# Optimization experiments

Hardware: AMD Instinct MI355X
Metric: run time of the kernel (lower is better)

Reference implementation:

```python
import jax, jax.numpy as jnp
import numpy as np
import math

N = 4096
D = 256


def _xavier(key, shape):
    fan_in, fan_out = shape[0], shape[1]
    std = math.sqrt(2.0 / (fan_in + fan_out))
    return jax.random.normal(key, shape, dtype=jnp.float32) * std


def setup_inputs() -> dict:
    key = jax.random.key(0)
    ks = jax.random.split(key, 12)
    return {
        "cur": jax.random.normal(ks[0], (N, D), dtype=jnp.float32),
        "pre": jax.random.normal(ks[1], (N, D), dtype=jnp.float32),
        # SpatialHyperedge params
        "r_proj_s": _xavier(ks[2], (D, D)),
        "incidence_s": _xavier(ks[3], (N, N - 1)),
        # TemporalHyperedge params
        "r_proj_t": _xavier(ks[4], (D, D)),
        "incidence_t": _xavier(ks[5], (N, N)),
        # HHNodeMP params
        "node_proj": _xavier(ks[6], (D, D)),
        "spa_edge_proj": _xavier(ks[7], (D, D)),
        "tmp_edge_proj": _xavier(ks[8], (D, D)),
        "theta_w": _xavier(ks[9], (D, D)),
        "theta_b": jnp.zeros((D,), dtype=jnp.float32),
    }


def _scatter_slave(vals):
    """Place [N, N-1] per-row slave values into a zero-diagonal [N, N] matrix.
    Row i's k-th slave is column k if k < i else k+1 (all j != i in order)."""
    n = vals.shape[0]
    k = jnp.arange(n - 1)[None, :]
    cols = k + (k >= jnp.arange(n)[:, None])  # [N, N-1] column indices
    rows = jnp.broadcast_to(jnp.arange(n)[:, None], (n, n - 1))
    return jnp.zeros((n, n), dtype=vals.dtype).at[rows.reshape(-1), cols.reshape(-1)].set(vals.reshape(-1))


def _fro(x):
    return jnp.sqrt(jnp.sum(x * x))


def reference(cur, pre, r_proj_s, incidence_s, r_proj_t, incidence_t,
              node_proj, spa_edge_proj, tmp_edge_proj, theta_w, theta_b):
    n, d = cur.shape
    inv_sqrt_d = 1.0 / math.sqrt(d)

    # ---- SpatialHyperedge ----
    Xd = jax.lax.stop_gradient(cur)
    master_s = Xd @ r_proj_s                                   # [N, D]
    M_s_full = _scatter_slave(incidence_s)                     # [N, N], zero diag
    neigh_recon_s = M_s_full @ Xd                              # == bmm over gathered slaves
    spatial_loss = (_fro(master_s - neigh_recon_s) * 0.2
                    + jnp.sum(jnp.abs(incidence_s))
                    + 0.001 * _fro(incidence_s))
    # clamp(min=0) then zero-out entries not strictly > 0  => relu-like
    clipped_s = jnp.where(incidence_s > 0.0, incidence_s, 0.0)
    incidence_all = _scatter_slave(clipped_s) + jnp.eye(n, dtype=cur.dtype)

    # ---- TemporalHyperedge ----
    cur_d = jax.lax.stop_gradient(cur)
    pre_d = jax.lax.stop_gradient(pre)
    master_t = cur_d @ r_proj_t
    neigh_recon_t = incidence_t @ pre_d
    temporal_loss = (_fro(master_t - neigh_recon_t) * 0.2
                     + jnp.sum(jnp.abs(incidence_t))
                     + 0.001 * _fro(incidence_t))
    incidence_t_clipped = jnp.maximum(incidence_t, 0.0)

    # ---- SpatialHyperedgeMP ----
    spa_edge_fea = incidence_all @ cur
    spa_deg = jnp.sum(incidence_all, axis=1, keepdims=True)
    spa_emb = spa_edge_fea / spa_deg                           # [N, D]

    # ---- TemporalHyperedgeMP ----
    tmp_edge_fea = incidence_t_clipped @ pre + cur
    tmp_deg = jnp.sum(incidence_t_clipped, axis=1, keepdims=True) + 1.0
    tmp_emb = tmp_edge_fea / tmp_deg                           # [N, D]

    # ---- HHNodeMP ----
    node_fea = cur @ node_proj
    spa_fea = spa_emb @ spa_edge_proj
    tmp_fea = tmp_emb @ tmp_edge_proj
    spa_attn = jnp.sum(spa_fea * node_fea, axis=1, keepdims=True) * inv_sqrt_d
    tmp_attn = jnp.sum(tmp_fea * node_fea, axis=1, keepdims=True) * inv_sqrt_d
    val = spa_attn * spa_fea + tmp_attn * tmp_fea
    node_emb = jax.nn.relu(val @ theta_w.T + theta_b)          # dropout = identity (eval)

    return node_emb, temporal_loss + spatial_loss
```

## Files before the change

### kernel.cpp

```cpp
#include <hip/hip_runtime.h>
#include <hip/hip_bf16.h>
#include <math.h>

#define NN 4096
#define DD 256

typedef __bf16 bf16x8 __attribute__((ext_vector_type(8)));
typedef short  short8 __attribute__((ext_vector_type(8)));
typedef float  f32x4  __attribute__((ext_vector_type(4)));

#define MFMA16(a, b, c) __builtin_amdgcn_mfma_f32_16x16x32_bf16((a), (b), (c), 0, 0, 0)

__device__ inline bf16x8 brelu(bf16x8 a) {
    short8 s = __builtin_bit_cast(short8, a);
    s = s & ~(s >> 15);
    return __builtin_bit_cast(bf16x8, s);
}

__device__ inline float wave_red(float v) {
#pragma unroll
    for (int o = 32; o > 0; o >>= 1) v += __shfl_down(v, o, 64);
    return v;
}

__device__ inline unsigned short bfbits(float f) {
    return __builtin_bit_cast(unsigned short, (__bf16)f);
}

__global__ __launch_bounds__(256) void k_prep(const float* __restrict__ cur,
                                              const float* __restrict__ pre,
                                              __bf16* __restrict__ cur_bf,
                                              __bf16* __restrict__ curT,
                                              __bf16* __restrict__ preT) {
    const int z = blockIdx.z;
    const int i0 = blockIdx.x * 64, d0 = blockIdx.y * 64;
    const float* src = z ? pre : cur;
    __bf16* dstT = z ? preT : curT;
    __shared__ unsigned short tile[64][72];
    const int t = threadIdx.x;
    const int r = t >> 2, c4 = (t & 3) * 16;
    const float* srow = src + (size_t)(i0 + r) * DD + d0 + c4;
    alignas(16) unsigned short loc[16];
#pragma unroll
    for (int e = 0; e < 4; ++e) {
        float4 v = ((const float4*)srow)[e];
        loc[e * 4 + 0] = bfbits(v.x);
        loc[e * 4 + 1] = bfbits(v.y);
        loc[e * 4 + 2] = bfbits(v.z);
        loc[e * 4 + 3] = bfbits(v.w);
    }
#pragma unroll
    for (int e = 0; e < 16; ++e) tile[r][c4 + e] = loc[e];
    if (z == 0) {
        __bf16* drow = cur_bf + (size_t)(i0 + r) * DD + d0 + c4;
        *(uint4*)drow = *(uint4*)&loc[0];
        *(uint4*)(drow + 8) = *(uint4*)&loc[8];
    }
    __syncthreads();
    alignas(16) unsigned short o[16];
#pragma unroll
    for (int e = 0; e < 16; ++e) o[e] = tile[c4 + e][r];
    __bf16* trow = dstT + (size_t)(d0 + r) * NN + i0 + c4;
    *(uint4*)trow = *(uint4*)&o[0];
    *(uint4*)(trow + 8) = *(uint4*)&o[8];
}

__global__ __launch_bounds__(256) void k_proj(
    const float* __restrict__ a0, const float* __restrict__ a1, const float* __restrict__ a2,
    const float* __restrict__ a3, const float* __restrict__ a4, const float* __restrict__ a5,
    __bf16* __restrict__ o0, __bf16* __restrict__ o1, __bf16* __restrict__ o2,
    __bf16* __restrict__ o3, __bf16* __restrict__ o4, __bf16* __restrict__ o5) {
    const int id = blockIdx.y, r = blockIdx.x, t = threadIdx.x;
    const float* src = id == 0 ? a0 : id == 1 ? a1 : id == 2 ? a2 : id == 3 ? a3 : id == 4 ? a4 : a5;
    __bf16* dst = id == 0 ? o0 : id == 1 ? o1 : id == 2 ? o2 : id == 3 ? o3 : id == 4 ? o4 : o5;
    float v = src[r * DD + t];
    if (id < 5) dst[t * DD + r] = (__bf16)v;
    else        dst[r * DD + t] = (__bf16)v;
}

__global__ __launch_bounds__(256) void k_conv_t(const float* __restrict__ inc,
                                                __bf16* __restrict__ Mbf,
                                                float* __restrict__ rowsum,
                                                float* __restrict__ pAbs, float* __restrict__ pSq) {
    const int i = blockIdx.x, t = threadIdx.x;
    const float4* src = (const float4*)(inc + (size_t)i * NN);
    ushort4* dst = (ushort4*)(Mbf + (size_t)i * NN);
    float rs = 0.f, as = 0.f, qs = 0.f;
#pragma unroll
    for (int e = 0; e < 4; ++e) {
        const int f = t + 256 * e;
        float4 v = src[f];
        float x[4] = {v.x, v.y, v.z, v.w};
        unsigned short o[4];
#pragma unroll
        for (int j = 0; j < 4; ++j) {
            float fv = x[j];
            as += fabsf(fv); qs += fv * fv; rs += fmaxf(fv, 0.f);
            o[j] = bfbits(fv);
        }
        dst[f] = make_ushort4(o[0], o[1], o[2], o[3]);
    }
    __shared__ float red[3][4];
    const int w = t >> 6, lane = t & 63;
    rs = wave_red(rs); as = wave_red(as); qs = wave_red(qs);
    if (lane == 0) { red[0][w] = rs; red[1][w] = as; red[2][w] = qs; }
    __syncthreads();
    if (t == 0) {
        rowsum[i] = red[0][0] + red[0][1] + red[0][2] + red[0][3];
        pAbs[i]   = red[1][0] + red[1][1] + red[1][2] + red[1][3];
        pSq[i]    = red[2][0] + red[2][1] + red[2][2] + red[2][3];
    }
}

__global__ __launch_bounds__(256) void k_conv_s(const float* __restrict__ inc,
                                                __bf16* __restrict__ Mbf,
                                                float* __restrict__ rowsum,
                                                float* __restrict__ pAbs, float* __restrict__ pSq) {
    const int i = blockIdx.x, t = threadIdx.x;
    __shared__ unsigned short row[NN];
    const float* srow = inc + (size_t)i * (NN - 1);
    float rs = 0.f, as = 0.f, qs = 0.f;
#pragma unroll
    for (int e = 0; e < 4; ++e) {
        const int f = t + 256 * e;
        float x[4] = {0.f, 0.f, 0.f, 0.f};
        if (f < 1023) __builtin_memcpy(x, srow + 4 * f, 16);
        else          __builtin_memcpy(x, srow + 4092, 12);
#pragma unroll
        for (int j = 0; j < 4; ++j) {
            const int k = 4 * f + j;
            float fv = x[j];
            as += fabsf(fv); qs += fv * fv; rs += fmaxf(fv, 0.f);
            if (k < NN - 1) row[k + (k >= i)] = bfbits(fv);
        }
    }
    if (t == 0) row[i] = 0;
    __syncthreads();
    uint4* dOut = (uint4*)(Mbf + (size_t)i * NN);
    const uint4* sIn = (const uint4*)row;
    dOut[t] = sIn[t];
    dOut[t + 256] = sIn[t + 256];
    __shared__ float red[3][4];
    const int w = t >> 6, lane = t & 63;
    rs = wave_red(rs); as = wave_red(as); qs = wave_red(qs);
    if (lane == 0) { red[0][w] = rs; red[1][w] = as; red[2][w] = qs; }
    __syncthreads();
    if (t == 0) {
        rowsum[i] = red[0][0] + red[0][1] + red[0][2] + red[0][3];
        pAbs[i]   = red[1][0] + red[1][1] + red[1][2] + red[1][3];
        pSq[i]    = red[2][0] + red[2][1] + red[2][2] + red[2][3];
    }
}

template <int DUAL>
__device__ inline void mfma_step(const __bf16 (&As)[64][72], const __bf16 (&Bs)[64][72],
                                 int wr, int wc, int quad, int l16,
                                 f32x4 (&accR)[2][2], f32x4 (&accL)[2][2]) {
#pragma unroll
    for (int ks = 0; ks < 2; ++ks) {
        const int kc = ks * 32 + quad * 8;
        bf16x8 a0 = *(const bf16x8*)&As[wr * 32 + l16][kc];
        bf16x8 a1 = *(const bf16x8*)&As[wr * 32 + 16 + l16][kc];
        bf16x8 b0 = *(const bf16x8*)&Bs[wc * 32 + l16][kc];
        bf16x8 b1 = *(const bf16x8*)&Bs[wc * 32 + 16 + l16][kc];
        accR[0][0] = MFMA16(a0, b0, accR[0][0]);
        accR[0][1] = MFMA16(a0, b1, accR[0][1]);
        accR[1][0] = MFMA16(a1, b0, accR[1][0]);
        accR[1][1] = MFMA16(a1, b1, accR[1][1]);
        if (DUAL) {
            bf16x8 a0r = brelu(a0), a1r = brelu(a1);
            accL[0][0] = MFMA16(a0r, b0, accL[0][0]);
            accL[0][1] = MFMA16(a0r, b1, accL[0][1]);
            accL[1][0] = MFMA16(a1r, b0, accL[1][0]);
            accL[1][1] = MFMA16(a1r, b1, accL[1][1]);
        }
    }
}

__global__ __launch_bounds__(256) void k_big(const __bf16* __restrict__ Mt, const __bf16* __restrict__ Ms,
                                             const __bf16* __restrict__ preT, const __bf16* __restrict__ curT,
                                             const float* __restrict__ negMt, const float* __restrict__ negMs,
                                             const float* __restrict__ cur,
                                             const float* __restrict__ rsT, const float* __restrict__ rsS,
                                             __bf16* __restrict__ embT, __bf16* __restrict__ embS,
                                             float* __restrict__ pDiff) {
    const int flat = blockIdx.x + 4 * (blockIdx.y + 64 * blockIdx.z);
    const int swz = (flat & 7) * 64 + (flat >> 3);
    const int bx = swz & 3, by = (swz >> 2) & 63, z = swz >> 8;
    const __bf16* A  = z ? Ms : Mt;
    const __bf16* BT = z ? curT : preT;
    const float* negM = z ? negMs : negMt;
    const float* rs   = z ? rsS : rsT;
    __bf16* emb       = z ? embS : embT;
    const int n0 = bx * 64, m0 = by * 64;
    __shared__ __bf16 As[2][64][72], Bs[2][64][72];
    __shared__ float sred[4];
    f32x4 accR[2][2], accL[2][2];
#pragma unroll
    for (int i = 0; i < 2; ++i)
#pragma unroll
        for (int j = 0; j < 2; ++j) { accR[i][j] = (f32x4)0.f; accL[i][j] = (f32x4)0.f; }
    const int t = threadIdx.x, w = t >> 6, lane = t & 63, quad = lane >> 4, l16 = lane & 15;
    const int wr = w >> 1, wc = w & 1;
    const int sr = t >> 2, sc = (t & 3) * 16;
    const __bf16* gA = A + (size_t)(m0 + sr) * NN + sc;
    const __bf16* gB = BT + (size_t)(n0 + sr) * NN + sc;
    uint4 av0 = *(const uint4*)(gA);
    uint4 av1 = *(const uint4*)(gA + 8);
    uint4 bv0 = *(const uint4*)(gB);
    uint4 bv1 = *(const uint4*)(gB + 8);
    gA += 64; gB += 64;
    *(uint4*)&As[0][sr][sc] = av0; *(uint4*)&As[0][sr][sc + 8] = av1;
    *(uint4*)&Bs[0][sr][sc] = bv0; *(uint4*)&Bs[0][sr][sc + 8] = bv1;
    av0 = *(const uint4*)(gA);
    av1 = *(const uint4*)(gA + 8);
    bv0 = *(const uint4*)(gB);
    bv1 = *(const uint4*)(gB + 8);
    gA += 64; gB += 64;
    __builtin_amdgcn_sched_barrier(0);
    asm volatile("s_waitcnt lgkmcnt(0)" ::: "memory");
    __builtin_amdgcn_s_barrier();
    int c = 0;
    for (int kt = 0; kt < NN / 64; ++kt) {
        __builtin_amdgcn_s_setprio(1);
        mfma_step<1>(As[c], Bs[c], wr, wc, quad, l16, accR, accL);
        __builtin_amdgcn_s_setprio(0);
        if (kt < NN / 64 - 1) {
            *(uint4*)&As[c ^ 1][sr][sc] = av0; *(uint4*)&As[c ^ 1][sr][sc + 8] = av1;
            *(uint4*)&Bs[c ^ 1][sr][sc] = bv0; *(uint4*)&Bs[c ^ 1][sr][sc + 8] = bv1;
            if (kt < NN / 64 - 2) {
                av0 = *(const uint4*)(gA);
                av1 = *(const uint4*)(gA + 8);
                bv0 = *(const uint4*)(gB);
                bv1 = *(const uint4*)(gB + 8);
                gA += 64; gB += 64;
            }
            __builtin_amdgcn_sched_barrier(0);
            asm volatile("s_waitcnt lgkmcnt(0)" ::: "memory");
        }
        __builtin_amdgcn_s_barrier();
        c ^= 1;
    }
    float sumd = 0.f;
#pragma unroll
    for (int mi = 0; mi < 2; ++mi)
#pragma unroll
        for (int ni = 0; ni < 2; ++ni)
#pragma unroll
            for (int r = 0; r < 4; ++r) {
                int gr = m0 + wr * 32 + mi * 16 + quad * 4 + r;
                int gc = n0 + wc * 32 + ni * 16 + l16;
                size_t idx = (size_t)gr * DD + gc;
                float diff = accR[mi][ni][r] + negM[idx];
                sumd += diff * diff;
                float inv = 1.f / (rs[gr] + 1.f);
                emb[idx] = (__bf16)((accL[mi][ni][r] + cur[idx]) * inv);
            }
    sumd = wave_red(sumd);
    if (lane == 0) sred[w] = sumd;
    __syncthreads();
    if (t == 0)
        pDiff[z * 256 + by * 4 + bx] = sred[0] + sred[1] + sred[2] + sred[3];
}

__global__ __launch_bounds__(256) void k_small3(const __bf16* __restrict__ cur_bf,
                                                const __bf16* __restrict__ pTs, const __bf16* __restrict__ pTt,
                                                const __bf16* __restrict__ pTn,
                                                float* __restrict__ negMs, float* __restrict__ negMt,
                                                float* __restrict__ nodeFea) {
    const int z = blockIdx.z;
    const __bf16* BT = z == 0 ? pTs : (z == 1 ? pTt : pTn);
    const int n0 = blockIdx.x * 64, m0 = blockIdx.y * 64;
    __shared__ __bf16 As[64][72], Bs[64][72];
    f32x4 accR[2][2];
#pragma unroll
    for (int i = 0; i < 2; ++i)
#pragma unroll
        for (int j = 0; j < 2; ++j) accR[i][j] = (f32x4)0.f;
    const int t = threadIdx.x, w = t >> 6, lane = t & 63, quad = lane >> 4, l16 = lane & 15;
    const int wr = w >> 1, wc = w & 1;
    const int sr = t >> 2, sc = (t & 3) * 16;
    const __bf16* gA = cur_bf + (size_t)(m0 + sr) * DD + sc;
    const __bf16* gB = BT + (size_t)(n0 + sr) * DD + sc;
    for (int kt = 0; kt < DD / 64; ++kt) {
        uint4 av0 = *(const uint4*)(gA);
        uint4 av1 = *(const uint4*)(gA + 8);
        uint4 bv0 = *(const uint4*)(gB);
        uint4 bv1 = *(const uint4*)(gB + 8);
        __syncthreads();
        *(uint4*)&As[sr][sc] = av0; *(uint4*)&As[sr][sc + 8] = av1;
        *(uint4*)&Bs[sr][sc] = bv0; *(uint4*)&Bs[sr][sc + 8] = bv1;
        __syncthreads();
        mfma_step<0>(As, Bs, wr, wc, quad, l16, accR, accR);
        gA += 64; gB += 64;
    }
#pragma unroll
    for (int mi = 0; mi < 2; ++mi)
#pragma unroll
        for (int ni = 0; ni < 2; ++ni)
#pragma unroll
            for (int r = 0; r < 4; ++r) {
                int gr = m0 + wr * 32 + mi * 16 + quad * 4 + r;
                int gc = n0 + wc * 32 + ni * 16 + l16;
                size_t idx = (size_t)gr * DD + gc;
                float v = accR[mi][ni][r];
                if (z == 0) negMs[idx] = -v;
                else if (z == 1) negMt[idx] = -v;
                else nodeFea[idx] = v;
            }
}

__global__ __launch_bounds__(256) void k_fea(const __bf16* __restrict__ embS, const __bf16* __restrict__ embT,
                                             const __bf16* __restrict__ pTspa, const __bf16* __restrict__ pTtmp,
                                             float* __restrict__ spaF, float* __restrict__ tmpF) {
    const int z = blockIdx.z;
    const __bf16* Ae = z ? embT : embS;
    const __bf16* BT = z ? pTtmp : pTspa;
    float* outF = z ? tmpF : spaF;
    const int n0 = blockIdx.x * 64, m0 = blockIdx.y * 64;
    __shared__ __bf16 As[64][72], Bs[64][72];
    f32x4 accR[2][2];
#pragma unroll
    for (int i = 0; i < 2; ++i)
#pragma unroll
        for (int j = 0; j < 2; ++j) accR[i][j] = (f32x4)0.f;
    const int t = threadIdx.x, w = t >> 6, lane = t & 63, quad = lane >> 4, l16 = lane & 15;
    const int wr = w >> 1, wc = w & 1;
    const int sr = t >> 2, sc = (t & 3) * 16;
    const __bf16* gA = Ae + (size_t)(m0 + sr) * DD + sc;
    const __bf16* gB = BT + (size_t)(n0 + sr) * DD + sc;
    for (int kt = 0; kt < DD / 64; ++kt) {
        uint4 av0 = *(const uint4*)(gA);
        uint4 av1 = *(const uint4*)(gA + 8);
        uint4 bv0 = *(const uint4*)(gB);
        uint4 bv1 = *(const uint4*)(gB + 8);
        __syncthreads();
        *(uint4*)&As[sr][sc] = av0; *(uint4*)&As[sr][sc + 8] = av1;
        *(uint4*)&Bs[sr][sc] = bv0; *(uint4*)&Bs[sr][sc + 8] = bv1;
        __syncthreads();
        mfma_step<0>(As, Bs, wr, wc, quad, l16, accR, accR);
        gA += 64; gB += 64;
    }
#pragma unroll
    for (int mi = 0; mi < 2; ++mi)
#pragma unroll
        for (int ni = 0; ni < 2; ++ni)
#pragma unroll
            for (int r = 0; r < 4; ++r) {
                int gr = m0 + wr * 32 + mi * 16 + quad * 4 + r;
                int gc = n0 + wc * 32 + ni * 16 + l16;
                outF[(size_t)gr * DD + gc] = accR[mi][ni][r];
            }
}

__global__ __launch_bounds__(256) void k_attn(const float* __restrict__ spaF, const float* __restrict__ tmpF,
                                              const float* __restrict__ nodeF,
                                              float* __restrict__ spaA, float* __restrict__ tmpA) {
    const int t = threadIdx.x, w = t >> 6, lane = t & 63;
    const int i = blockIdx.x * 4 + w;
    const float4* sf = (const float4*)(spaF + (size_t)i * DD);
    const float4* tf = (const float4*)(tmpF + (size_t)i * DD);
    const float4* nf = (const float4*)(nodeF + (size_t)i * DD);
    float4 s = sf[lane], p = tf[lane], n = nf[lane];
    float ds = s.x * n.x + s.y * n.y + s.z * n.z + s.w * n.w;
    float dt = p.x * n.x + p.y * n.y + p.z * n.z + p.w * n.w;
    ds = wave_red(ds); dt = wave_red(dt);
    if (lane == 0) { spaA[i] = ds * 0.0625f; tmpA[i] = dt * 0.0625f; }
}

__global__ __launch_bounds__(256) void k_final(const float* __restrict__ spaF, const float* __restrict__ tmpF,
                                               const float* __restrict__ spaA, const float* __restrict__ tmpA,
                                               const __bf16* __restrict__ thetaBf, const float* __restrict__ thetaB,
                                               float* __restrict__ out) {
    const int n0 = blockIdx.x * 64, m0 = blockIdx.y * 64;
    __shared__ __bf16 As[64][72], Bs[64][72];
    f32x4 accR[2][2];
#pragma unroll
    for (int i = 0; i < 2; ++i)
#pragma unroll
        for (int j = 0; j < 2; ++j) accR[i][j] = (f32x4)0.f;
    const int t = threadIdx.x, w = t >> 6, lane = t & 63, quad = lane >> 4, l16 = lane & 15;
    const int wr = w >> 1, wc = w & 1;
    const int sr = t >> 2, sc = (t & 3) * 16;
    const float sa = spaA[m0 + sr], ta = tmpA[m0 + sr];
    const float* gS = spaF + (size_t)(m0 + sr) * DD + sc;
    const float* gT = tmpF + (size_t)(m0 + sr) * DD + sc;
    const __bf16* gB = thetaBf + (size_t)(n0 + sr) * DD + sc;
    for (int kt = 0; kt < DD / 64; ++kt) {
        __bf16 tmp[16];
#pragma unroll
        for (int e4 = 0; e4 < 4; ++e4) {
            float4 vs = ((const float4*)gS)[e4];
            float4 vt = ((const float4*)gT)[e4];
            tmp[e4 * 4 + 0] = (__bf16)(sa * vs.x + ta * vt.x);
            tmp[e4 * 4 + 1] = (__bf16)(sa * vs.y + ta * vt.y);
            tmp[e4 * 4 + 2] = (__bf16)(sa * vs.z + ta * vt.z);
            tmp[e4 * 4 + 3] = (__bf16)(sa * vs.w + ta * vt.w);
        }
        uint4 bv0 = *(const uint4*)(gB);
        uint4 bv1 = *(const uint4*)(gB + 8);
        __syncthreads();
        *(uint4*)&As[sr][sc] = *(uint4*)&tmp[0]; *(uint4*)&As[sr][sc + 8] = *(uint4*)&tmp[8];
        *(uint4*)&Bs[sr][sc] = bv0; *(uint4*)&Bs[sr][sc + 8] = bv1;
        __syncthreads();
        mfma_step<0>(As, Bs, wr, wc, quad, l16, accR, accR);
        gS += 64; gT += 64; gB += 64;
    }
#pragma unroll
    for (int mi = 0; mi < 2; ++mi)
#pragma unroll
        for (int ni = 0; ni < 2; ++ni)
#pragma unroll
            for (int r = 0; r < 4; ++r) {
                int gr = m0 + wr * 32 + mi * 16 + quad * 4 + r;
                int gc = n0 + wc * 32 + ni * 16 + l16;
                float v = accR[mi][ni][r] + thetaB[gc];
                out[(size_t)gr * DD + gc] = fmaxf(v, 0.f);
            }
}

__global__ __launch_bounds__(256) void k_loss(const float* __restrict__ pAbsT, const float* __restrict__ pSqT,
                                              const float* __restrict__ pAbsS, const float* __restrict__ pSqS,
                                              const float* __restrict__ pDiff,
                                              float* __restrict__ out) {
    const int t = threadIdx.x;
    float aT = 0.f, qT = 0.f, aS = 0.f, qS = 0.f;
#pragma unroll
    for (int j = 0; j < 16; ++j) {
        const int i = t + 256 * j;
        aT += pAbsT[i]; qT += pSqT[i]; aS += pAbsS[i]; qS += pSqS[i];
    }
    float dT = pDiff[t], dS = pDiff[256 + t];
    aT = wave_red(aT); qT = wave_red(qT); aS = wave_red(aS); qS = wave_red(qS);
    dT = wave_red(dT); dS = wave_red(dS);
    __shared__ float red[6][4];
    const int w = t >> 6, lane = t & 63;
    if (lane == 0) { red[0][w] = aT; red[1][w] = qT; red[2][w] = aS; red[3][w] = qS; red[4][w] = dT; red[5][w] = dS; }
    __syncthreads();
    if (t == 0) {
        float s[6];
#pragma unroll
        for (int k = 0; k < 6; ++k) s[k] = red[k][0] + red[k][1] + red[k][2] + red[k][3];
        float l = s[0] + 0.001f * sqrtf(s[1]) + 0.2f * sqrtf(s[4])
                + s[2] + 0.001f * sqrtf(s[3]) + 0.2f * sqrtf(s[5]);
        out[(size_t)NN * DD] = l;
    }
}

extern "C" void kernel_launch(void* const* d_in, const int* in_sizes, int n_in,
                              void* d_out, int out_size, void* d_ws, size_t ws_size,
                              hipStream_t stream) {
    (void)in_sizes; (void)n_in; (void)out_size; (void)ws_size;
    const float* cur      = (const float*)d_in[0];
    const float* pre      = (const float*)d_in[1];
    const float* r_proj_s = (const float*)d_in[2];
    const float* inc_s    = (const float*)d_in[3];
    const float* r_proj_t = (const float*)d_in[4];
    const float* inc_t    = (const float*)d_in[5];
    const float* node_pj  = (const float*)d_in[6];
    const float* spa_pj   = (const float*)d_in[7];
    const float* tmp_pj   = (const float*)d_in[8];
    const float* theta_w  = (const float*)d_in[9];
    const float* theta_b  = (const float*)d_in[10];
    float* out = (float*)d_out;

    char* p = (char*)d_ws;
    auto alloc = [&](size_t bytes) -> void* {
        void* r = (void*)p;
        p += (bytes + 255) & ~(size_t)255;
        return r;
    };
    __bf16* Mt      = (__bf16*)alloc((size_t)NN * NN * 2);
    __bf16* Ms      = (__bf16*)alloc((size_t)NN * NN * 2);
    __bf16* cur_bf  = (__bf16*)alloc((size_t)NN * DD * 2);
    __bf16* curT    = (__bf16*)alloc((size_t)NN * DD * 2);
    __bf16* preT    = (__bf16*)alloc((size_t)NN * DD * 2);
    __bf16* pTs     = (__bf16*)alloc((size_t)DD * DD * 2);
    __bf16* pTt     = (__bf16*)alloc((size_t)DD * DD * 2);
    __bf16* pTn     = (__bf16*)alloc((size_t)DD * DD * 2);
    __bf16* pTspa   = (__bf16*)alloc((size_t)DD * DD * 2);
    __bf16* pTtmp   = (__bf16*)alloc((size_t)DD * DD * 2);
    __bf16* thetaBf = (__bf16*)alloc((size_t)DD * DD * 2);
    __bf16* embS    = (__bf16*)alloc((size_t)NN * DD * 2);
    __bf16* embT    = (__bf16*)alloc((size_t)NN * DD * 2);
    float* negMs    = (float*)alloc((size_t)NN * DD * 4);
    float* negMt    = (float*)alloc((size_t)NN * DD * 4);
    float* nodeFea  = (float*)alloc((size_t)NN * DD * 4);
    float* spaF     = (float*)alloc((size_t)NN * DD * 4);
    float* tmpF     = (float*)alloc((size_t)NN * DD * 4);
    float* rsS      = (float*)alloc((size_t)NN * 4);
    float* rsT      = (float*)alloc((size_t)NN * 4);
    float* spaA     = (float*)alloc((size_t)NN * 4);
    float* tmpA     = (float*)alloc((size_t)NN * 4);
    float* pAbsT    = (float*)alloc((size_t)NN * 4);
    float* pSqT     = (float*)alloc((size_t)NN * 4);
    float* pAbsS    = (float*)alloc((size_t)NN * 4);
    float* pSqS     = (float*)alloc((size_t)NN * 4);
    float* pDiff    = (float*)alloc(512 * 4);

    k_prep<<<dim3(NN / 64, DD / 64, 2), 256, 0, stream>>>(cur, pre, cur_bf, curT, preT);
    k_proj<<<dim3(DD, 6), 256, 0, stream>>>(r_proj_s, r_proj_t, node_pj, spa_pj, tmp_pj, theta_w,
                                            pTs, pTt, pTn, pTspa, pTtmp, thetaBf);
    k_conv_t<<<NN, 256, 0, stream>>>(inc_t, Mt, rsT, pAbsT, pSqT);
    k_conv_s<<<NN, 256, 0, stream>>>(inc_s, Ms, rsS, pAbsS, pSqS);
    k_small3<<<dim3(4, 64, 3), 256, 0, stream>>>(cur_bf, pTs, pTt, pTn, negMs, negMt, nodeFea);
    k_big<<<dim3(4, 64, 2), 256, 0, stream>>>(Mt, Ms, preT, curT, negMt, negMs, cur,
                                              rsT, rsS, embT, embS, pDiff);
    k_fea<<<dim3(4, 64, 2), 256, 0, stream>>>(embS, embT, pTspa, pTtmp, spaF, tmpF);
    k_attn<<<NN / 4, 256, 0, stream>>>(spaF, tmpF, nodeFea, spaA, tmpA);
    k_final<<<dim3(4, 64), 256, 0, stream>>>(spaF, tmpF, spaA, tmpA, thetaBf, theta_b, out);
    k_loss<<<1, 256, 0, stream>>>(pAbsT, pSqT, pAbsS, pSqS, pDiff, out);
}
```

Measured before the change: 262.2 us.

## Use direct global-to-LDS loads with XOR swizzle in k_big; fuse attention dot into k_fea

The main big GEMM kernel now stages A/B tiles via global_load_lds directly into an XOR-swizzled, unpadded LDS buffer. It prefetches two tiles ahead with vmcnt-based waits and reads fragments into registers before issuing the next stage. This removes register staging and the ds_write traffic in the K loop. Separately, the attention dot products are computed in the k_fea epilogue as per-slice partial sums reduced in k_final, which eliminates the k_attn launch and its reread of spaF, tmpF and nodeFea.

```diff
diff --git a/kernel.cpp b/kernel.cpp
--- a/kernel.cpp
+++ b/kernel.cpp
@@ -8,6 +8,10 @@
 typedef __bf16 bf16x8 __attribute__((ext_vector_type(8)));
 typedef short  short8 __attribute__((ext_vector_type(8)));
 typedef float  f32x4  __attribute__((ext_vector_type(4)));
+
+typedef __attribute__((address_space(1))) const void gv_t;
+typedef __attribute__((address_space(3))) void lv_t;
+#define GLD16(gp, lp) __builtin_amdgcn_global_load_lds((gv_t*)(gp), (lv_t*)(lp), 16, 0, 0)
 
 #define MFMA16(a, b, c) __builtin_amdgcn_mfma_f32_16x16x32_bf16((a), (b), (c), 0, 0, 0)
 
@@ -152,10 +156,9 @@
     }
 }
 
-template <int DUAL>
-__device__ inline void mfma_step(const __bf16 (&As)[64][72], const __bf16 (&Bs)[64][72],
-                                 int wr, int wc, int quad, int l16,
-                                 f32x4 (&accR)[2][2], f32x4 (&accL)[2][2]) {
+__device__ inline void mfma_step_s(const __bf16 (&As)[64][72], const __bf16 (&Bs)[64][72],
+                                   int wr, int wc, int quad, int l16,
+                                   f32x4 (&accR)[2][2]) {
 #pragma unroll
     for (int ks = 0; ks < 2; ++ks) {
         const int kc = ks * 32 + quad * 8;
@@ -167,13 +170,6 @@
         accR[0][1] = MFMA16(a0, b1, accR[0][1]);
         accR[1][0] = MFMA16(a1, b0, accR[1][0]);
         accR[1][1] = MFMA16(a1, b1, accR[1][1]);
-        if (DUAL) {
-            bf16x8 a0r = brelu(a0), a1r = brelu(a1);
-            accL[0][0] = MFMA16(a0r, b0, accL[0][0]);
-            accL[0][1] = MFMA16(a0r, b1, accL[0][1]);
-            accL[1][0] = MFMA16(a1r, b0, accL[1][0]);
-            accL[1][1] = MFMA16(a1r, b1, accL[1][1]);
-        }
     }
 }
 
@@ -193,7 +189,7 @@
     const float* rs   = z ? rsS : rsT;
     __bf16* emb       = z ? embS : embT;
     const int n0 = bx * 64, m0 = by * 64;
-    __shared__ __bf16 As[2][64][72], Bs[2][64][72];
+    __shared__ __bf16 sm[2][2][64][64];
     __shared__ float sred[4];
     f32x4 accR[2][2], accL[2][2];
 #pragma unroll
@@ -202,43 +198,66 @@
         for (int j = 0; j < 2; ++j) { accR[i][j] = (f32x4)0.f; accL[i][j] = (f32x4)0.f; }
     const int t = threadIdx.x, w = t >> 6, lane = t & 63, quad = lane >> 4, l16 = lane & 15;
     const int wr = w >> 1, wc = w & 1;
-    const int sr = t >> 2, sc = (t & 3) * 16;
-    const __bf16* gA = A + (size_t)(m0 + sr) * NN + sc;
-    const __bf16* gB = BT + (size_t)(n0 + sr) * NN + sc;
-    uint4 av0 = *(const uint4*)(gA);
-    uint4 av1 = *(const uint4*)(gA + 8);
-    uint4 bv0 = *(const uint4*)(gB);
-    uint4 bv1 = *(const uint4*)(gB + 8);
-    gA += 64; gB += 64;
-    *(uint4*)&As[0][sr][sc] = av0; *(uint4*)&As[0][sr][sc + 8] = av1;
-    *(uint4*)&Bs[0][sr][sc] = bv0; *(uint4*)&Bs[0][sr][sc + 8] = bv1;
-    av0 = *(const uint4*)(gA);
-    av1 = *(const uint4*)(gA + 8);
-    bv0 = *(const uint4*)(gB);
-    bv1 = *(const uint4*)(gB + 8);
-    gA += 64; gB += 64;
+    const int lr = lane >> 3, lc = lane & 7;
+    const int q0 = 2 * w, q1 = q0 + 1;
+    const int csw = ((lc ^ lr) * 8);
+    const __bf16* gA0 = A + (size_t)(m0 + 8 * q0 + lr) * NN + csw;
+    const __bf16* gA1 = A + (size_t)(m0 + 8 * q1 + lr) * NN + csw;
+    const __bf16* gB0 = BT + (size_t)(n0 + 8 * q0 + lr) * NN + csw;
+    const __bf16* gB1 = BT + (size_t)(n0 + 8 * q1 + lr) * NN + csw;
+    auto stage = [&](int b, int tk) {
+        const int ko = tk * 64;
+        GLD16(gA0 + ko, &sm[b][0][8 * q0][0]);
+        GLD16(gA1 + ko, &sm[b][0][8 * q1][0]);
+        GLD16(gB0 + ko, &sm[b][1][8 * q0][0]);
+        GLD16(gB1 + ko, &sm[b][1][8 * q1][0]);
+    };
+    stage(0, 0);
+    stage(1, 1);
+    asm volatile("s_waitcnt vmcnt(4)" ::: "memory");
+    __builtin_amdgcn_s_barrier();
     __builtin_amdgcn_sched_barrier(0);
-    asm volatile("s_waitcnt lgkmcnt(0)" ::: "memory");
-    __builtin_amdgcn_s_barrier();
+    const int h8 = l16 & 7;
+    const int ra0 = wr * 32 + l16, ra1 = ra0 + 16;
+    const int rb0 = wc * 32 + l16, rb1 = rb0 + 16;
     int c = 0;
-    for (int kt = 0; kt < NN / 64; ++kt) {
+    const int NT = NN / 64;
+    for (int kt = 0; kt < NT; ++kt) {
+        bf16x8 a0k[2], a1k[2], b0k[2], b1k[2];
+#pragma unroll
+        for (int ks = 0; ks < 2; ++ks) {
+            const int sw = ((4 * ks + quad) ^ h8) * 8;
+            a0k[ks] = *(const bf16x8*)&sm[c][0][ra0][sw];
+            a1k[ks] = *(const bf16x8*)&sm[c][0][ra1][sw];
+            b0k[ks] = *(const bf16x8*)&sm[c][1][rb0][sw];
+            b1k[ks] = *(const bf16x8*)&sm[c][1][rb1][sw];
+        }
+        asm volatile("s_waitcnt lgkmcnt(0)" ::: "memory");
+        __builtin_amdgcn_sched_barrier(0);
+        __builtin_amdgcn_s_barrier();
+        __builtin_amdgcn_sched_barrier(0);
+        if (kt < NT - 2) stage(c, kt + 2);
+        __builtin_amdgcn_sched_barrier(0);
         __builtin_amdgcn_s_setprio(1);
-        mfma_step<1>(As[c], Bs[c], wr, wc, quad, l16, accR, accL);
+#pragma unroll
+        for (int ks = 0; ks < 2; ++ks) {
+            accR[0][0] = MFMA16(a0k[ks], b0k[ks], accR[0][0]);
+            accR[0][1] = MFMA16(a0k[ks], b1k[ks], accR[0][1]);
+            accR[1][0] = MFMA16(a1k[ks], b0k[ks], accR[1][0]);
+            accR[1][1] = MFMA16(a1k[ks], b1k[ks], accR[1][1]);
+            bf16x8 a0r = brelu(a0k[ks]), a1r = brelu(a1k[ks]);
+            accL[0][0] = MFMA16(a0r, b0k[ks], accL[0][0]);
+            accL[0][1] = MFMA16(a0r, b1k[ks], accL[0][1]);
+            accL[1][0] = MFMA16(a1r, b0k[ks], accL[1][0]);
+            accL[1][1] = MFMA16(a1r, b1k[ks], accL[1][1]);
+        }
         __builtin_amdgcn_s_setprio(0);
-        if (kt < NN / 64 - 1) {
-            *(uint4*)&As[c ^ 1][sr][sc] = av0; *(uint4*)&As[c ^ 1][sr][sc + 8] = av1;
-            *(uint4*)&Bs[c ^ 1][sr][sc] = bv0; *(uint4*)&Bs[c ^ 1][sr][sc + 8] = bv1;
-            if (kt < NN / 64 - 2) {
-                av0 = *(const uint4*)(gA);
-                av1 = *(const uint4*)(gA + 8);
-                bv0 = *(const uint4*)(gB);
-                bv1 = *(const uint4*)(gB + 8);
-                gA += 64; gB += 64;
-            }
+        if (kt < NT - 1) {
+            if (kt < NT - 2) asm volatile("s_waitcnt vmcnt(4)" ::: "memory");
+            else             asm volatile("s_waitcnt vmcnt(0)" ::: "memory");
+            __builtin_amdgcn_s_barrier();
             __builtin_amdgcn_sched_barrier(0);
-            asm volatile("s_waitcnt lgkmcnt(0)" ::: "memory");
-        }
-        __builtin_amdgcn_s_barrier();
+        }
         c ^= 1;
     }
     float sumd = 0.f;
@@ -291,7 +310,7 @@
         *(uint4*)&As[sr][sc] = av0; *(uint4*)&As[sr][sc + 8] = av1;
         *(uint4*)&Bs[sr][sc] = bv0; *(uint4*)&Bs[sr][sc + 8] = bv1;
         __syncthreads();
-        mfma_step<0>(As, Bs, wr, wc, quad, l16, accR, accR);
+        mfma_step_s(As, Bs, wr, wc, quad, l16, accR);
         gA += 64; gB += 64;
     }
 #pragma unroll
@@ -312,11 +331,14 @@
 
 __global__ __launch_bounds__(256) void k_fea(const __bf16* __restrict__ embS, const __bf16* __restrict__ embT,
                                              const __bf16* __restrict__ pTspa, const __bf16* __restrict__ pTtmp,
-                                             float* __restrict__ spaF, float* __restrict__ tmpF) {
+                                             const float* __restrict__ nodeF,
+                                             float* __restrict__ spaF, float* __restrict__ tmpF,
+                                             float* __restrict__ pSpa, float* __restrict__ pTmp) {
     const int z = blockIdx.z;
     const __bf16* Ae = z ? embT : embS;
     const __bf16* BT = z ? pTtmp : pTspa;
     float* outF = z ? tmpF : spaF;
+    float* pOut = z ? pTmp : pSpa;
     const int n0 = blockIdx.x * 64, m0 = blockIdx.y * 64;
     __shared__ __bf16 As[64][72], Bs[64][72];
     f32x4 accR[2][2];
@@ -338,38 +360,34 @@
         *(uint4*)&As[sr][sc] = av0; *(uint4*)&As[sr][sc + 8] = av1;
         *(uint4*)&Bs[sr][sc] = bv0; *(uint4*)&Bs[sr][sc + 8] = bv1;
         __syncthreads();
-        mfma_step<0>(As, Bs, wr, wc, quad, l16, accR, accR);
+        mfma_step_s(As, Bs, wr, wc, quad, l16, accR);
         gA += 64; gB += 64;
     }
+    const int slice = blockIdx.x * 2 + wc;
 #pragma unroll
     for (int mi = 0; mi < 2; ++mi)
 #pragma unroll
-        for (int ni = 0; ni < 2; ++ni)
-#pragma unroll
-            for (int r = 0; r < 4; ++r) {
-                int gr = m0 + wr * 32 + mi * 16 + quad * 4 + r;
-                int gc = n0 + wc * 32 + ni * 16 + l16;
-                outF[(size_t)gr * DD + gc] = accR[mi][ni][r];
+        for (int r = 0; r < 4; ++r) {
+            const int gr = m0 + wr * 32 + mi * 16 + quad * 4 + r;
+            float s = 0.f;
+#pragma unroll
+            for (int ni = 0; ni < 2; ++ni) {
+                const int gc = n0 + wc * 32 + ni * 16 + l16;
+                const size_t idx = (size_t)gr * DD + gc;
+                const float v = accR[mi][ni][r];
+                outF[idx] = v;
+                s += v * nodeF[idx];
             }
-}
-
-__global__ __launch_bounds__(256) void k_attn(const float* __restrict__ spaF, const float* __restrict__ tmpF,
-                                              const float* __restrict__ nodeF,
-                                              float* __restrict__ spaA, float* __restrict__ tmpA) {
-    const int t = threadIdx.x, w = t >> 6, lane = t & 63;
-    const int i = blockIdx.x * 4 + w;
-    const float4* sf = (const float4*)(spaF + (size_t)i * DD);
-    const float4* tf = (const float4*)(tmpF + (size_t)i * DD);
-    const float4* nf = (const float4*)(nodeF + (size_t)i * DD);
-    float4 s = sf[lane], p = tf[lane], n = nf[lane];
-    float ds = s.x * n.x + s.y * n.y + s.z * n.z + s.w * n.w;
-    float dt = p.x * n.x + p.y * n.y + p.z * n.z + p.w * n.w;
-    ds = wave_red(ds); dt = wave_red(dt);
-    if (lane == 0) { spaA[i] = ds * 0.0625f; tmpA[i] = dt * 0.0625f; }
+            s += __shfl_xor(s, 1, 64);
+            s += __shfl_xor(s, 2, 64);
+            s += __shfl_xor(s, 4, 64);
+            s += __shfl_xor(s, 8, 64);
+            if (l16 == 0) pOut[(size_t)slice * NN + gr] = s;
+        }
 }
 
 __global__ __launch_bounds__(256) void k_final(const float* __restrict__ spaF, const float* __restrict__ tmpF,
-                                               const float* __restrict__ spaA, const float* __restrict__ tmpA,
+                                               const float* __restrict__ pSpa, const float* __restrict__ pTmp,
                                                const __bf16* __restrict__ thetaBf, const float* __restrict__ thetaB,
                                                float* __restrict__ out) {
     const int n0 = blockIdx.x * 64, m0 = blockIdx.y * 64;
@@ -382,9 +400,16 @@
     const int t = threadIdx.x, w = t >> 6, lane = t & 63, quad = lane >> 4, l16 = lane & 15;
     const int wr = w >> 1, wc = w & 1;
     const int sr = t >> 2, sc = (t & 3) * 16;
-    const float sa = spaA[m0 + sr], ta = tmpA[m0 + sr];
-    const float* gS = spaF + (size_t)(m0 + sr) * DD + sc;
-    const float* gT = tmpF + (size_t)(m0 + sr) * DD + sc;
+    const int row = m0 + sr;
+    float sa = 0.f, ta = 0.f;
+#pragma unroll
+    for (int j = 0; j < 8; ++j) {
+        sa += pSpa[(size_t)j * NN + row];
+        ta += pTmp[(size_t)j * NN + row];
+    }
+    sa *= 0.0625f; ta *= 0.0625f;
+    const float* gS = spaF + (size_t)row * DD + sc;
+    const float* gT = tmpF + (size_t)row * DD + sc;
     const __bf16* gB = thetaBf + (size_t)(n0 + sr) * DD + sc;
     for (int kt = 0; kt < DD / 64; ++kt) {
         __bf16 tmp[16];
@@ -403,7 +428,7 @@
         *(uint4*)&As[sr][sc] = *(uint4*)&tmp[0]; *(uint4*)&As[sr][sc + 8] = *(uint4*)&tmp[8];
         *(uint4*)&Bs[sr][sc] = bv0; *(uint4*)&Bs[sr][sc + 8] = bv1;
         __syncthreads();
-        mfma_step<0>(As, Bs, wr, wc, quad, l16, accR, accR);
+        mfma_step_s(As, Bs, wr, wc, quad, l16, accR);
         gS += 64; gT += 64; gB += 64;
     }
 #pragma unroll
@@ -490,8 +515,8 @@
     float* tmpF     = (float*)alloc((size_t)NN * DD * 4);
     float* rsS      = (float*)alloc((size_t)NN * 4);
     float* rsT      = (float*)alloc((size_t)NN * 4);
-    float* spaA     = (float*)alloc((size_t)NN * 4);
-    float* tmpA     = (float*)alloc((size_t)NN * 4);
+    float* pSpa     = (float*)alloc((size_t)8 * NN * 4);
+    float* pTmp     = (float*)alloc((size_t)8 * NN * 4);
     float* pAbsT    = (float*)alloc((size_t)NN * 4);
     float* pSqT     = (float*)alloc((size_t)NN * 4);
     float* pAbsS    = (float*)alloc((size_t)NN * 4);
@@ -506,8 +531,8 @@
     k_small3<<<dim3(4, 64, 3), 256, 0, stream>>>(cur_bf, pTs, pTt, pTn, negMs, negMt, nodeFea);
     k_big<<<dim3(4, 64, 2), 256, 0, stream>>>(Mt, Ms, preT, curT, negMt, negMs, cur,
                                               rsT, rsS, embT, embS, pDiff);
-    k_fea<<<dim3(4, 64, 2), 256, 0, stream>>>(embS, embT, pTspa, pTtmp, spaF, tmpF);
-    k_attn<<<NN / 4, 256, 0, stream>>>(spaF, tmpF, nodeFea, spaA, tmpA);
-    k_final<<<dim3(4, 64), 256, 0, stream>>>(spaF, tmpF, spaA, tmpA, thetaBf, theta_b, out);
+    k_fea<<<dim3(4, 64, 2), 256, 0, stream>>>(embS, embT, pTspa, pTtmp, nodeFea,
+                                              spaF, tmpF, pSpa, pTmp);
+    k_final<<<dim3(4, 64), 256, 0, stream>>>(spaF, tmpF, pSpa, pTmp, thetaBf, theta_b, out);
     k_loss<<<1, 256, 0, stream>>>(pAbsT, pSqT, pAbsS, pSqS, pDiff, out);
 }
```

Result: faster. 255.3 us (-2.6%).
